# Kernel tuning notes

Hardware: AMD Instinct MI355X
Metric: run time of the kernel (lower is better)

The kernel has to match this reference:

```python
import jax, jax.numpy as jnp
import numpy as np
from jax import lax

# VGG16 conv config: (in_ch, out_ch) for 13 3x3 convs; maxpool after layer idx in _POOL_AFTER
_CFG = [(3,64),(64,64),(64,128),(128,128),(128,256),(256,256),(256,256),(256,512),(512,512),(512,512),(512,512),(512,512),(512,512)]
_POOL_AFTER = {1,3,6,9,12}
NUM_CLASSES, START, V, E, H, B, T = 20, 20, 22, 64, 512, 8, 20


def _conv_relu(x, w, b):
    y = lax.conv_general_dilated(x, w, (1,1), 'SAME', dimension_numbers=('NCHW','OIHW','NCHW'))
    return jax.nn.relu(y + b[None, :, None, None])


def _maxpool2(x):
    return lax.reduce_window(x, -jnp.inf, lax.max, (1,1,2,2), (1,1,2,2), 'VALID')


def setup_inputs() -> dict:
    key = jax.random.key(0)
    ks = jax.random.split(key, 64)
    ctr = [0]
    def rn(shape, fan_in):
        k = ks[ctr[0]]; ctr[0] += 1
        return jax.random.normal(k, shape, jnp.float32) * np.float32(1.0/np.sqrt(fan_in))
    inp = {}
    for i, (cin, cout) in enumerate(_CFG):
        inp['w%d' % (i+1)] = rn((cout, cin, 3, 3), cin*9)
        inp['b%d' % (i+1)] = jnp.zeros((cout,), jnp.float32)
    inp['fc1_w'] = rn((4096, 25088), 25088); inp['fc1_b'] = jnp.zeros((4096,), jnp.float32)
    inp['fc2_w'] = rn((4096, 4096), 4096);   inp['fc2_b'] = jnp.zeros((4096,), jnp.float32)
    inp['embed_W'] = rn((V, E), E)
    inp['w_ih'] = rn((4*H, E), E); inp['w_hh'] = rn((4*H, H), H)
    inp['b_ih'] = jnp.zeros((4*H,), jnp.float32); inp['b_hh'] = jnp.zeros((4*H,), jnp.float32)
    inp['proj_rnn_w'] = rn((E, H), H);    inp['proj_rnn_b'] = jnp.zeros((E,), jnp.float32)
    inp['proj_img_w'] = rn((E, 4096), 4096); inp['proj_img_b'] = jnp.zeros((E,), jnp.float32)
    inp['images'] = jax.random.normal(ks[ctr[0]], (B, 3, 224, 224), jnp.float32); ctr[0] += 1
    inp['tokens'] = jax.random.randint(ks[ctr[0]], (B, T), 0, NUM_CLASSES, dtype=jnp.int32)
    return inp


def reference(w1, b1, w2, b2, w3, b3, w4, b4, w5, b5, w6, b6, w7, b7, w8, b8, w9, b9, w10, b10, w11, b11, w12, b12, w13, b13,
              fc1_w, fc1_b, fc2_w, fc2_b, embed_W, w_ih, w_hh, b_ih, b_hh,
              proj_rnn_w, proj_rnn_b, proj_img_w, proj_img_b, images, tokens):
    ws = [w1,w2,w3,w4,w5,w6,w7,w8,w9,w10,w11,w12,w13]
    bs = [b1,b2,b3,b4,b5,b6,b7,b8,b9,b10,b11,b12,b13]
    # ---- extract_img: VGG16 features + (identity 7x7 avgpool) + classifier[:-2], eval-mode dropout = identity ----
    x = images
    for i in range(13):
        x = _conv_relu(x, ws[i], bs[i])
        if i in _POOL_AFTER:
            x = _maxpool2(x)
    f = x.reshape(x.shape[0], -1)                         # [B, 25088]
    f = jax.nn.relu(f @ fc1_w.T + fc1_b)
    f = jax.nn.relu(f @ fc2_w.T + fc2_b)                  # [B, 4096]
    img_emb = f @ proj_img_w.T + proj_img_b               # [B, E]  (proj_img, dropout=identity)
    # ---- get_W: embedding weights with START row masked to -1e9 ----
    Wsc = embed_W.at[START].set(-1e9)
    # ---- per-step decode (teacher forced): embed -> LSTM -> relu(proj_rnn + img_emb) -> scores -> log_softmax ----
    Bn = tokens.shape[0]
    inp_tok = jnp.concatenate([jnp.full((Bn, 1), START, tokens.dtype), tokens[:, :-1]], axis=1)
    emb = embed_W[inp_tok]                                # [B, T, E]
    bias = b_ih + b_hh
    def step(carry, e_t):
        h, c = carry
        g = e_t @ w_ih.T + h @ w_hh.T + bias              # [B, 4H], torch gate order i,f,g,o
        i_, f_, g_, o_ = jnp.split(g, 4, axis=-1)
        c = jax.nn.sigmoid(f_) * c + jax.nn.sigmoid(i_) * jnp.tanh(g_)
        h = jax.nn.sigmoid(o_) * jnp.tanh(c)
        return (h, c), h
    h0 = jnp.zeros((Bn, H), jnp.float32)
    _, hs = lax.scan(step, (h0, h0), emb.transpose(1, 0, 2))   # [T, B, H]
    xdec = jax.nn.relu(hs @ proj_rnn_w.T + proj_rnn_b + img_emb[None])  # [T, B, E]
    scores = xdec @ Wsc.T                                 # [T, B, V]
    logp = jax.nn.log_softmax(scores, axis=-1)
    return logp.transpose(1, 0, 2)                        # [B, T, V]
```

## Files before the change

kernel.cpp:

```cpp
#include <hip/hip_runtime.h>
#include <math.h>

#define BATCH 8
#define T_STEPS 20
#define VOCAB 22
#define EDIM 64
#define HDIM 512
#define START_TOK 20

#define KC 8

__global__ __launch_bounds__(256) void transpose_w_kernel(
    const float* __restrict__ w, float* __restrict__ wt, int Cin, int Cout)
{
    size_t total = (size_t)Cout * Cin * 9;
    size_t idx = (size_t)blockIdx.x * 256 + threadIdx.x;
    if (idx >= total) return;
    int o = (int)(idx % Cout);
    size_t rest = idx / Cout;
    int tap = (int)(rest % 9);
    int ic = (int)(rest / 9);
    wt[idx] = w[((size_t)o * Cin + ic) * 9 + tap];
}

template<int TYG, int TXG>
__global__ __launch_bounds__(256, 2) void conv_reg_kernel(
    const float* __restrict__ x, const float* __restrict__ wt,
    const float* __restrict__ bias, float* __restrict__ y,
    int Cin, int Cout, int H, int W, int tiles_c, int ks, int cper)
{
    constexpr int TR = 4 * TYG;
    constexpr int TC = 4 * TXG;
    constexpr int XR = TR + 2;
    constexpr int XC = TC + 2;

    int tile = blockIdx.x;
    int tr = tile / tiles_c, tc = tile - tr * tiles_c;
    int r0 = tr * TR, c0 = tc * TC;
    int nb = blockIdx.z;
    int ksi = nb % ks;
    int n = nb / ks;
    int ob = blockIdx.y * 64;
    int tx = threadIdx.x % TXG;
    int ty = (threadIdx.x / TXG) % TYG;
    int tz = threadIdx.x >> 4;

    __shared__ float xs[KC][XR][XC];
    __shared__ float wsh[KC][9][64];

    float acc[4][4][4];
    #pragma unroll
    for (int r = 0; r < 4; ++r)
        #pragma unroll
        for (int c = 0; c < 4; ++c)
            #pragma unroll
            for (int j = 0; j < 4; ++j) acc[r][c][j] = 0.f;

    const float* xn = x + (size_t)n * Cin * H * W;
    int ic_beg = ksi * cper;

    for (int ic0 = ic_beg; ic0 < ic_beg + cper; ic0 += KC) {
        for (int idx = threadIdx.x; idx < KC * XR * XC; idx += 256) {
            int lc = idx % XC;
            int rest = idx / XC;
            int lr = rest % XR;
            int i = rest / XR;
            int gr = r0 - 1 + lr, gc = c0 - 1 + lc;
            float v = 0.f;
            if ((unsigned)gr < (unsigned)H && (unsigned)gc < (unsigned)W)
                v = xn[((size_t)(ic0 + i) * H + gr) * W + gc];
            xs[i][lr][lc] = v;
        }
        for (int idx = threadIdx.x; idx < KC * 9 * 64; idx += 256) {
            int o = idx & 63;
            int rest = idx >> 6;
            int tap = rest % 9;
            int i = rest / 9;
            wsh[i][tap][o] = wt[((size_t)(ic0 + i) * 9 + tap) * Cout + ob + o];
        }
        __syncthreads();

        #pragma unroll 2
        for (int i = 0; i < KC; ++i) {
            float xv[6][6];
            #pragma unroll
            for (int rr = 0; rr < 6; ++rr) {
                #pragma unroll
                for (int jj = 0; jj < 3; ++jj) {
                    float2 t = *(const float2*)&xs[i][4 * ty + rr][4 * tx + 2 * jj];
                    xv[rr][2 * jj]     = t.x;
                    xv[rr][2 * jj + 1] = t.y;
                }
            }
            #pragma unroll
            for (int kh = 0; kh < 3; ++kh) {
                #pragma unroll
                for (int kw = 0; kw < 3; ++kw) {
                    float4 wv = *(const float4*)&wsh[i][kh * 3 + kw][tz * 4];
                    #pragma unroll
                    for (int r = 0; r < 4; ++r) {
                        #pragma unroll
                        for (int c = 0; c < 4; ++c) {
                            float xvv = xv[r + kh][c + kw];
                            acc[r][c][0] = fmaf(xvv, wv.x, acc[r][c][0]);
                            acc[r][c][1] = fmaf(xvv, wv.y, acc[r][c][1]);
                            acc[r][c][2] = fmaf(xvv, wv.z, acc[r][c][2]);
                            acc[r][c][3] = fmaf(xvv, wv.w, acc[r][c][3]);
                        }
                    }
                }
            }
        }
        __syncthreads();
    }

    int row0 = r0 + 4 * ty;
    int col0 = c0 + 4 * tx;
    if (col0 >= W) return;
    float4 bv = make_float4(0.f, 0.f, 0.f, 0.f);
    if (ks == 1) bv = *(const float4*)&bias[ob + tz * 4];
    bool full4 = (col0 + 3 < W);
    #pragma unroll
    for (int r = 0; r < 4; ++r) {
        int row = row0 + r;
        if (row >= H) continue;
        size_t rbase = (size_t)row * W + col0;
        #pragma unroll
        for (int j = 0; j < 4; ++j) {
            int o = ob + tz * 4 + j;
            float bj = (j == 0) ? bv.x : (j == 1) ? bv.y : (j == 2) ? bv.z : bv.w;
            float* yo = y + ((size_t)nb * Cout + o) * ((size_t)H * W) + rbase;
            float v0 = acc[r][0][j] + bj;
            float v1 = acc[r][1][j] + bj;
            float v2 = acc[r][2][j] + bj;
            float v3 = acc[r][3][j] + bj;
            if (ks == 1) {
                v0 = fmaxf(v0, 0.f); v1 = fmaxf(v1, 0.f);
                v2 = fmaxf(v2, 0.f); v3 = fmaxf(v3, 0.f);
            }
            if (full4 && ((rbase & 3) == 0)) {
                *(float4*)yo = make_float4(v0, v1, v2, v3);
            } else {
                yo[0] = v0;
                if (col0 + 1 < W) yo[1] = v1;
                if (col0 + 2 < W) yo[2] = v2;
                if (col0 + 3 < W) yo[3] = v3;
            }
        }
    }
}

__global__ __launch_bounds__(256) void ksum_kernel(
    const float* __restrict__ part, const float* __restrict__ bias,
    float* __restrict__ y, int ks, int Cout, int HW)
{
    size_t total = (size_t)BATCH * Cout * HW;
    size_t i = (size_t)blockIdx.x * 256 + threadIdx.x;
    if (i >= total) return;
    int sp = (int)(i % HW);
    size_t r = i / HW;
    int o = (int)(r % Cout);
    int n = (int)(r / Cout);
    float s = 0.f;
    for (int k = 0; k < ks; ++k)
        s += part[(((size_t)(n * ks + k) * Cout + o) * HW) + sp];
    y[i] = fmaxf(s + bias[o], 0.f);
}

__global__ __launch_bounds__(256) void conv3x3_relu_kernel(
    const float* __restrict__ x, const float* __restrict__ w,
    const float* __restrict__ bias, float* __restrict__ y,
    int Cin, int Cout, int Hs, int Ws)
{
    int HW = Hs * Ws;
    int sp = blockIdx.x * 256 + threadIdx.x;
    if (sp >= HW) return;
    int h = sp / Ws;
    int col = sp - h * Ws;
    int o = blockIdx.y;
    int n = blockIdx.z;
    const float* xn = x + (size_t)n * Cin * HW;
    const float* wo = w + (size_t)o * Cin * 9;
    float acc = bias[o];
    if (h >= 1 && h < Hs - 1 && col >= 1 && col < Ws - 1) {
        const float* xr = xn + (size_t)(h - 1) * Ws + (col - 1);
        for (int i = 0; i < Cin; ++i) {
            const float* xc = xr + (size_t)i * HW;
            const float* wc = wo + i * 9;
            acc += xc[0] * wc[0] + xc[1] * wc[1] + xc[2] * wc[2];
            acc += xc[Ws] * wc[3] + xc[Ws + 1] * wc[4] + xc[Ws + 2] * wc[5];
            acc += xc[2 * Ws] * wc[6] + xc[2 * Ws + 1] * wc[7] + xc[2 * Ws + 2] * wc[8];
        }
    } else {
        for (int i = 0; i < Cin; ++i) {
            const float* xc = xn + (size_t)i * HW;
            const float* wc = wo + i * 9;
            #pragma unroll
            for (int kh = 0; kh < 3; ++kh) {
                int hh = h + kh - 1;
                if (hh < 0 || hh >= Hs) continue;
                #pragma unroll
                for (int kw = 0; kw < 3; ++kw) {
                    int cc = col + kw - 1;
                    if (cc < 0 || cc >= Ws) continue;
                    acc += xc[hh * Ws + cc] * wc[kh * 3 + kw];
                }
            }
        }
    }
    y[((size_t)n * Cout + o) * HW + sp] = fmaxf(acc, 0.f);
}

__global__ __launch_bounds__(256) void maxpool2_kernel(
    const float* __restrict__ x, float* __restrict__ y, int C, int Hin, int Win)
{
    int Ho = Hin >> 1, Wo = Win >> 1;
    size_t total = (size_t)BATCH * C * Ho * Wo;
    size_t i = (size_t)blockIdx.x * 256 + threadIdx.x;
    if (i >= total) return;
    int wo = (int)(i % Wo);
    size_t r = i / Wo;
    int ho = (int)(r % Ho);
    r /= Ho;
    const float* xp = x + (r * Hin + 2 * (size_t)ho) * Win + 2 * wo;
    float m = fmaxf(fmaxf(xp[0], xp[1]), fmaxf(xp[Win], xp[Win + 1]));
    y[i] = m;
}

__global__ __launch_bounds__(256) void linear8_kernel(
    const float* __restrict__ X, const float* __restrict__ W,
    const float* __restrict__ bias, float* __restrict__ Y,
    int K, int O, int doRelu)
{
    int o = blockIdx.x;
    const float* wr = W + (size_t)o * K;
    float acc[BATCH];
    #pragma unroll
    for (int b = 0; b < BATCH; ++b) acc[b] = 0.f;
    for (int k = threadIdx.x; k < K; k += 256) {
        float wv = wr[k];
        #pragma unroll
        for (int b = 0; b < BATCH; ++b)
            acc[b] = fmaf(X[(size_t)b * K + k], wv, acc[b]);
    }
    __shared__ float red[4][BATCH];
    int lane = threadIdx.x & 63, wid = threadIdx.x >> 6;
    #pragma unroll
    for (int b = 0; b < BATCH; ++b) {
        float v = acc[b];
        #pragma unroll
        for (int off = 32; off > 0; off >>= 1) v += __shfl_down(v, off, 64);
        if (lane == 0) red[wid][b] = v;
    }
    __syncthreads();
    if (threadIdx.x < BATCH) {
        float v = red[0][threadIdx.x] + red[1][threadIdx.x] +
                  red[2][threadIdx.x] + red[3][threadIdx.x];
        v += bias[o];
        if (doRelu) v = fmaxf(v, 0.f);
        Y[(size_t)threadIdx.x * O + o] = v;
    }
}

__global__ __launch_bounds__(256) void zero_kernel(float* __restrict__ p, int n)
{
    int i = blockIdx.x * 256 + threadIdx.x;
    if (i < n) p[i] = 0.f;
}

__global__ __launch_bounds__(256) void lstm_step_kernel(
    const float* __restrict__ embed_W, const int* __restrict__ tokens,
    const float* __restrict__ w_ih, const float* __restrict__ w_hh,
    const float* __restrict__ b_ih, const float* __restrict__ b_hh,
    const float* __restrict__ h_in, const float* __restrict__ c_in,
    float* __restrict__ h_out, float* __restrict__ c_out, int t)
{
    int idx = blockIdx.x * 256 + threadIdx.x;
    int b = idx >> 9;
    int j = idx & (HDIM - 1);
    int tok = (t == 0) ? START_TOK : tokens[b * T_STEPS + (t - 1)];
    const float* e = embed_W + (size_t)tok * EDIM;
    const float* hb = h_in + (size_t)b * HDIM;
    float g[4];
    #pragma unroll
    for (int q = 0; q < 4; ++q) {
        int row = q * HDIM + j;
        float a = b_ih[row] + b_hh[row];
        const float* wi = w_ih + (size_t)row * EDIM;
        for (int k = 0; k < EDIM; ++k) a = fmaf(e[k], wi[k], a);
        const float* wh = w_hh + (size_t)row * HDIM;
        for (int k = 0; k < HDIM; ++k) a = fmaf(hb[k], wh[k], a);
        g[q] = a;
    }
    float ig = 1.f / (1.f + expf(-g[0]));
    float fg = 1.f / (1.f + expf(-g[1]));
    float gg = tanhf(g[2]);
    float og = 1.f / (1.f + expf(-g[3]));
    float c = fg * c_in[idx] + ig * gg;
    float h = og * tanhf(c);
    c_out[idx] = c;
    h_out[idx] = h;
}

__global__ __launch_bounds__(64) void decode_kernel(
    const float* __restrict__ hs, const float* __restrict__ proj_rnn_w,
    const float* __restrict__ proj_rnn_b, const float* __restrict__ img_emb,
    const float* __restrict__ embed_W, float* __restrict__ out)
{
    int bid = blockIdx.x;
    int t = bid >> 3;
    int b = bid & 7;
    int e = threadIdx.x;
    const float* hrow = hs + ((size_t)t * BATCH + b) * HDIM;
    float a = proj_rnn_b[e] + img_emb[b * EDIM + e];
    const float* wr = proj_rnn_w + (size_t)e * HDIM;
    for (int k = 0; k < HDIM; ++k) a = fmaf(hrow[k], wr[k], a);
    a = fmaxf(a, 0.f);
    __shared__ float xdec[EDIM];
    __shared__ float sc[VOCAB];
    xdec[e] = a;
    __syncthreads();
    if (e < VOCAB) {
        float s = 0.f;
        if (e == START_TOK) {
            for (int k = 0; k < EDIM; ++k) s += xdec[k];
            s *= -1e9f;
        } else {
            const float* w2 = embed_W + (size_t)e * EDIM;
            for (int k = 0; k < EDIM; ++k) s = fmaf(xdec[k], w2[k], s);
        }
        sc[e] = s;
    }
    __syncthreads();
    if (e == 0) {
        float m = -INFINITY;
        for (int v = 0; v < VOCAB; ++v) m = fmaxf(m, sc[v]);
        float sum = 0.f;
        for (int v = 0; v < VOCAB; ++v) sum += expf(sc[v] - m);
        float lse = m + logf(sum);
        for (int v = 0; v < VOCAB; ++v)
            out[((size_t)b * T_STEPS + t) * VOCAB + v] = sc[v] - lse;
    }
}

static const int CIN_[13]  = {3, 64, 64, 128, 128, 256, 256, 256, 512, 512, 512, 512, 512};
static const int COUT_[13] = {64, 64, 128, 128, 256, 256, 256, 512, 512, 512, 512, 512, 512};
static const int HSZ_[13]  = {224, 224, 112, 112, 56, 56, 56, 28, 28, 28, 14, 14, 14};
static const bool POOL_[13] = {false, true, false, true, false, false, true,
                               false, false, true, false, false, true};
static const int KS_[13]   = {1, 1, 1, 1, 1, 1, 1, 2, 2, 2, 8, 8, 8};

extern "C" void kernel_launch(void* const* d_in, const int* in_sizes, int n_in,
                              void* d_out, int out_size, void* d_ws, size_t ws_size,
                              hipStream_t stream) {
    const float* fc1_w = (const float*)d_in[26];
    const float* fc1_b = (const float*)d_in[27];
    const float* fc2_w = (const float*)d_in[28];
    const float* fc2_b = (const float*)d_in[29];
    const float* embed_W = (const float*)d_in[30];
    const float* w_ih = (const float*)d_in[31];
    const float* w_hh = (const float*)d_in[32];
    const float* b_ih = (const float*)d_in[33];
    const float* b_hh = (const float*)d_in[34];
    const float* proj_rnn_w = (const float*)d_in[35];
    const float* proj_rnn_b = (const float*)d_in[36];
    const float* proj_img_w = (const float*)d_in[37];
    const float* proj_img_b = (const float*)d_in[38];
    const float* images = (const float*)d_in[39];
    const int* tokens = (const int*)d_in[40];
    float* out = (float*)d_out;

    char* p = (char*)d_ws;
    auto alloc = [&](size_t nbytes) -> float* {
        float* r = (float*)p;
        p += (nbytes + 255) & ~(size_t)255;
        return r;
    };
    const size_t MAXACT = (size_t)BATCH * 64 * 224 * 224;
    float* bufs[2];
    bufs[0] = alloc(MAXACT * 4);
    bufs[1] = alloc(MAXACT * 4);
    float* f1 = alloc((size_t)BATCH * 4096 * 4);
    float* f2 = alloc((size_t)BATCH * 4096 * 4);
    float* img_emb = alloc((size_t)BATCH * EDIM * 4);
    float* zeros = alloc((size_t)BATCH * HDIM * 4);
    float* cbuf = alloc((size_t)BATCH * HDIM * 4);
    float* hs = alloc((size_t)T_STEPS * BATCH * HDIM * 4);
    float* wt = alloc((size_t)512 * 9 * 512 * 4);

    int di = 0;
    const float* cur = images;
    for (int i = 0; i < 13; ++i) {
        int Hs = HSZ_[i], Ws = Hs, HW = Hs * Ws;
        float* dst = bufs[di]; di ^= 1;
        if (i == 0) {
            dim3 grid((HW + 255) / 256, COUT_[i], BATCH);
            conv3x3_relu_kernel<<<grid, 256, 0, stream>>>(
                cur, (const float*)d_in[0], (const float*)d_in[1], dst,
                CIN_[i], COUT_[i], Hs, Ws);
        } else {
            size_t wtotal = (size_t)COUT_[i] * CIN_[i] * 9;
            transpose_w_kernel<<<(int)((wtotal + 255) / 256), 256, 0, stream>>>(
                (const float*)d_in[2 * i], wt, CIN_[i], COUT_[i]);
            int ks = KS_[i];
            int cper = CIN_[i] / ks;
            float* tgt = (ks == 1) ? dst : (dst + (size_t)8 * 1024 * 1024);
            if (Hs == 56) {
                int tiles_r = (Hs + 7) / 8, tiles_c = (Ws + 31) / 32;
                dim3 grid(tiles_r * tiles_c, COUT_[i] / 64, BATCH * ks);
                conv_reg_kernel<2, 8><<<grid, 256, 0, stream>>>(
                    cur, wt, (const float*)d_in[2 * i + 1], tgt,
                    CIN_[i], COUT_[i], Hs, Ws, tiles_c, ks, cper);
            } else {
                int tiles_r = (Hs + 15) / 16, tiles_c = (Ws + 15) / 16;
                dim3 grid(tiles_r * tiles_c, COUT_[i] / 64, BATCH * ks);
                conv_reg_kernel<4, 4><<<grid, 256, 0, stream>>>(
                    cur, wt, (const float*)d_in[2 * i + 1], tgt,
                    CIN_[i], COUT_[i], Hs, Ws, tiles_c, ks, cper);
            }
            if (ks > 1) {
                size_t total = (size_t)BATCH * COUT_[i] * HW;
                ksum_kernel<<<(int)((total + 255) / 256), 256, 0, stream>>>(
                    tgt, (const float*)d_in[2 * i + 1], dst, ks, COUT_[i], HW);
            }
        }
        cur = dst;
        if (POOL_[i]) {
            float* pdst = bufs[di]; di ^= 1;
            size_t total = (size_t)BATCH * COUT_[i] * (Hs / 2) * (Ws / 2);
            maxpool2_kernel<<<(int)((total + 255) / 256), 256, 0, stream>>>(
                cur, pdst, COUT_[i], Hs, Ws);
            cur = pdst;
        }
    }

    linear8_kernel<<<4096, 256, 0, stream>>>(cur, fc1_w, fc1_b, f1, 25088, 4096, 1);
    linear8_kernel<<<4096, 256, 0, stream>>>(f1, fc2_w, fc2_b, f2, 4096, 4096, 1);
    linear8_kernel<<<64, 256, 0, stream>>>(f2, proj_img_w, proj_img_b, img_emb, 4096, 64, 0);

    zero_kernel<<<16, 256, 0, stream>>>(zeros, BATCH * HDIM);
    for (int t = 0; t < T_STEPS; ++t) {
        const float* h_in = (t == 0) ? zeros : (hs + (size_t)(t - 1) * BATCH * HDIM);
        const float* c_in = (t == 0) ? zeros : cbuf;
        lstm_step_kernel<<<16, 256, 0, stream>>>(
            embed_W, tokens, w_ih, w_hh, b_ih, b_hh,
            h_in, c_in, hs + (size_t)t * BATCH * HDIM, cbuf, t);
    }

    decode_kernel<<<T_STEPS * BATCH, 64, 0, stream>>>(
        hs, proj_rnn_w, proj_rnn_b, img_emb, embed_W, out);
}
```

Before: 7.018 ms.

## Double-buffer conv tiles via direct global-to-LDS loads with zero-page padding

Rewrites the conv tile staging to use AMD global_load_lds so data goes from global memory straight into LDS, and double-buffers the input and weight tiles so the next channel chunk loads while the current one is computed. Out-of-bounds halo elements are read from a small zeroed page instead of being branched to zero. KC is halved to 4 and launch bounds raised to 4 blocks per CU so the doubled shared-memory footprint still allows higher occupancy. The risks are register pressure from the precomputed offsets under the tighter occupancy target, and per-wave LDS destination layout assumptions of the direct-load instruction.

```diff
diff --git a/kernel.cpp b/kernel.cpp
--- a/kernel.cpp
+++ b/kernel.cpp
@@ -8,7 +8,17 @@
 #define HDIM 512
 #define START_TOK 20
 
-#define KC 8
+#define KC 4
+
+typedef __attribute__((address_space(1))) const void* as1cv;
+typedef __attribute__((address_space(3))) void* as3v;
+
+__device__ __forceinline__ void gload_lds4(const float* g, float* l) {
+    __builtin_amdgcn_global_load_lds((as1cv)g, (as3v)l, 4, 0, 0);
+}
+__device__ __forceinline__ void gload_lds16(const float* g, float* l) {
+    __builtin_amdgcn_global_load_lds((as1cv)g, (as3v)l, 16, 0, 0);
+}
 
 __global__ __launch_bounds__(256) void transpose_w_kernel(
     const float* __restrict__ w, float* __restrict__ wt, int Cin, int Cout)
@@ -24,15 +34,24 @@
 }
 
 template<int TYG, int TXG>
-__global__ __launch_bounds__(256, 2) void conv_reg_kernel(
+__global__ __launch_bounds__(256, 4) void conv_reg_kernel(
     const float* __restrict__ x, const float* __restrict__ wt,
     const float* __restrict__ bias, float* __restrict__ y,
+    const float* __restrict__ zpage,
     int Cin, int Cout, int H, int W, int tiles_c, int ks, int cper)
 {
     constexpr int TR = 4 * TYG;
     constexpr int TC = 4 * TXG;
     constexpr int XR = TR + 2;
     constexpr int XC = TC + 2;
+    constexpr int XN = KC * XR * XC;
+    constexpr int XIT = (XN + 255) / 256;
+    constexpr int WROWS = KC * 9;
+    constexpr int WQ = WROWS * 16;
+    constexpr int WIT = (WQ + 255) / 256;
+
+    __shared__ float xs[2][XN];
+    __shared__ float wsh[2][WROWS * 64];
 
     int tile = blockIdx.x;
     int tr = tile / tiles_c, tc = tile - tr * tiles_c;
@@ -41,12 +60,58 @@
     int ksi = nb % ks;
     int n = nb / ks;
     int ob = blockIdx.y * 64;
-    int tx = threadIdx.x % TXG;
-    int ty = (threadIdx.x / TXG) % TYG;
-    int tz = threadIdx.x >> 4;
-
-    __shared__ float xs[KC][XR][XC];
-    __shared__ float wsh[KC][9][64];
+    int tid = threadIdx.x;
+    int tx = tid % TXG;
+    int ty = (tid / TXG) % TYG;
+    int tz = tid >> 4;
+    int wid = tid >> 6;
+
+    int xoff[XIT];
+    unsigned xvalid = 0;
+    #pragma unroll
+    for (int it = 0; it < XIT; ++it) {
+        int idx = it * 256 + tid;
+        int i = idx / (XR * XC);
+        int rem = idx - i * (XR * XC);
+        int lr = rem / XC;
+        int lc = rem - lr * XC;
+        int gr = r0 - 1 + lr, gc = c0 - 1 + lc;
+        bool v = (idx < XN) && ((unsigned)gr < (unsigned)H) && ((unsigned)gc < (unsigned)W);
+        xoff[it] = (i * H + gr) * W + gc;
+        if (v) xvalid |= (1u << it);
+    }
+    int woff[WIT];
+    #pragma unroll
+    for (int it = 0; it < WIT; ++it) {
+        int idx = it * 256 + tid;
+        int row = idx >> 4;
+        int o4 = (idx & 15) * 4;
+        woff[it] = row * Cout + ob + o4;
+    }
+
+    const float* xn_ = x + (size_t)n * Cin * H * W;
+    int ic_beg = ksi * cper;
+    int nch = cper / KC;
+
+    auto stage = [&](int buf, int ic0) {
+        const float* xc = xn_ + (size_t)ic0 * H * W;
+        #pragma unroll
+        for (int it = 0; it < XIT; ++it) {
+            int idx = it * 256 + tid;
+            if (idx < XN) {
+                const float* src = ((xvalid >> it) & 1) ? (xc + xoff[it]) : zpage;
+                gload_lds4(src, &xs[buf][it * 256 + wid * 64]);
+            }
+        }
+        const float* wc = wt + (size_t)ic0 * 9 * Cout;
+        #pragma unroll
+        for (int it = 0; it < WIT; ++it) {
+            int idx = it * 256 + tid;
+            if (idx < WQ) {
+                gload_lds16(wc + woff[it], &wsh[buf][(it * 256 + wid * 64) * 4]);
+            }
+        }
+    };
 
     float acc[4][4][4];
     #pragma unroll
@@ -56,30 +121,14 @@
             #pragma unroll
             for (int j = 0; j < 4; ++j) acc[r][c][j] = 0.f;
 
-    const float* xn = x + (size_t)n * Cin * H * W;
-    int ic_beg = ksi * cper;
-
-    for (int ic0 = ic_beg; ic0 < ic_beg + cper; ic0 += KC) {
-        for (int idx = threadIdx.x; idx < KC * XR * XC; idx += 256) {
-            int lc = idx % XC;
-            int rest = idx / XC;
-            int lr = rest % XR;
-            int i = rest / XR;
-            int gr = r0 - 1 + lr, gc = c0 - 1 + lc;
-            float v = 0.f;
-            if ((unsigned)gr < (unsigned)H && (unsigned)gc < (unsigned)W)
-                v = xn[((size_t)(ic0 + i) * H + gr) * W + gc];
-            xs[i][lr][lc] = v;
-        }
-        for (int idx = threadIdx.x; idx < KC * 9 * 64; idx += 256) {
-            int o = idx & 63;
-            int rest = idx >> 6;
-            int tap = rest % 9;
-            int i = rest / 9;
-            wsh[i][tap][o] = wt[((size_t)(ic0 + i) * 9 + tap) * Cout + ob + o];
-        }
-        __syncthreads();
-
+    stage(0, ic_beg);
+    __syncthreads();
+
+    int cur = 0;
+    for (int c = 0; c < nch; ++c) {
+        if (c + 1 < nch) stage(cur ^ 1, ic_beg + (c + 1) * KC);
+        const float* xb = &xs[cur][0];
+        const float* wb = &wsh[cur][0];
         #pragma unroll 2
         for (int i = 0; i < KC; ++i) {
             float xv[6][6];
@@ -87,7 +136,7 @@
             for (int rr = 0; rr < 6; ++rr) {
                 #pragma unroll
                 for (int jj = 0; jj < 3; ++jj) {
-                    float2 t = *(const float2*)&xs[i][4 * ty + rr][4 * tx + 2 * jj];
+                    float2 t = *(const float2*)&xb[(i * XR + 4 * ty + rr) * XC + 4 * tx + 2 * jj];
                     xv[rr][2 * jj]     = t.x;
                     xv[rr][2 * jj + 1] = t.y;
                 }
@@ -96,22 +145,23 @@
             for (int kh = 0; kh < 3; ++kh) {
                 #pragma unroll
                 for (int kw = 0; kw < 3; ++kw) {
-                    float4 wv = *(const float4*)&wsh[i][kh * 3 + kw][tz * 4];
+                    float4 wv = *(const float4*)&wb[(i * 9 + kh * 3 + kw) * 64 + tz * 4];
                     #pragma unroll
                     for (int r = 0; r < 4; ++r) {
                         #pragma unroll
-                        for (int c = 0; c < 4; ++c) {
-                            float xvv = xv[r + kh][c + kw];
-                            acc[r][c][0] = fmaf(xvv, wv.x, acc[r][c][0]);
-                            acc[r][c][1] = fmaf(xvv, wv.y, acc[r][c][1]);
-                            acc[r][c][2] = fmaf(xvv, wv.z, acc[r][c][2]);
-                            acc[r][c][3] = fmaf(xvv, wv.w, acc[r][c][3]);
+                        for (int cc = 0; cc < 4; ++cc) {
+                            float xvv = xv[r + kh][cc + kw];
+                            acc[r][cc][0] = fmaf(xvv, wv.x, acc[r][cc][0]);
+                            acc[r][cc][1] = fmaf(xvv, wv.y, acc[r][cc][1]);
+                            acc[r][cc][2] = fmaf(xvv, wv.z, acc[r][cc][2]);
+                            acc[r][cc][3] = fmaf(xvv, wv.w, acc[r][cc][3]);
                         }
                     }
                 }
             }
         }
         __syncthreads();
+        cur ^= 1;
     }
 
     int row0 = r0 + 4 * ty;
@@ -387,6 +437,9 @@
     float* cbuf = alloc((size_t)BATCH * HDIM * 4);
     float* hs = alloc((size_t)T_STEPS * BATCH * HDIM * 4);
     float* wt = alloc((size_t)512 * 9 * 512 * 4);
+    float* zpage = alloc(256);
+
+    zero_kernel<<<1, 256, 0, stream>>>(zpage, 64);
 
     int di = 0;
     const float* cur = images;
@@ -409,13 +462,13 @@
                 int tiles_r = (Hs + 7) / 8, tiles_c = (Ws + 31) / 32;
                 dim3 grid(tiles_r * tiles_c, COUT_[i] / 64, BATCH * ks);
                 conv_reg_kernel<2, 8><<<grid, 256, 0, stream>>>(
-                    cur, wt, (const float*)d_in[2 * i + 1], tgt,
+                    cur, wt, (const float*)d_in[2 * i + 1], tgt, zpage,
                     CIN_[i], COUT_[i], Hs, Ws, tiles_c, ks, cper);
             } else {
                 int tiles_r = (Hs + 15) / 16, tiles_c = (Ws + 15) / 16;
                 dim3 grid(tiles_r * tiles_c, COUT_[i] / 64, BATCH * ks);
                 conv_reg_kernel<4, 4><<<grid, 256, 0, stream>>>(
-                    cur, wt, (const float*)d_in[2 * i + 1], tgt,
+                    cur, wt, (const float*)d_in[2 * i + 1], tgt, zpage,
                     CIN_[i], COUT_[i], Hs, Ws, tiles_c, ks, cper);
             }
             if (ks > 1) {
```

Result: slower. 8.051 ms (+14.7%).
